# Optimization experiments

Hardware: AMD Instinct MI355X
Metric: run time of the kernel (lower is better)

The kernel has to match this reference:

```python
import jax, jax.numpy as jnp
import numpy as np

NUM_FIELDS = 32


def setup_inputs() -> dict:
    key = jax.random.key(0)
    x = jax.random.normal(key, (16384, NUM_FIELDS, 64), dtype=jnp.float32)
    return {"x": x}


def reference(x) -> jnp.ndarray:
    # x: [B, N, D] == list of N tensors [B,1,D] stacked on dim 1.
    # Original: for all i<j pairs, sum_d x[:,i,:]*x[:,j,:] -> [B, N(N-1)/2, 1].
    # Equivalent efficient form: Gram matrix x @ x^T, take strict upper triangle.
    n = x.shape[1]
    gram = jnp.einsum('bnd,bmd->bnm', x, x)  # [B, N, N]
    rows, cols = jnp.triu_indices(n, k=1)    # pair order matches i<j double loop
    inner_product = gram[:, rows, cols][..., None]  # [B, N(N-1)/2, 1]
    return inner_product
```

## Files before the change

### kernel.cpp

```cpp
#include <hip/hip_runtime.h>
#include <hip/hip_bf16.h>

#define NFIELDS 32
#define DDIM 64
#define NPAIR 496

typedef __attribute__((ext_vector_type(8))) __bf16 bf16x8;
typedef __attribute__((ext_vector_type(4))) float f32x4;

__device__ __forceinline__ int pair_idx(int i, int j) {
    return i * 31 - (i * (i - 1)) / 2 + (j - i - 1);
}

__global__ __launch_bounds__(256) void inner_product_kernel(
        const float* __restrict__ x, float* __restrict__ out, int nbatch) {
    const int gtid = blockIdx.x * blockDim.x + threadIdx.x;
    const int wave = gtid >> 6;
    const int lane = threadIdx.x & 63;
    if (wave >= nbatch) return;

    const float* xb = x + (size_t)wave * (NFIELDS * DDIM);
    const int r = lane & 15;
    const int g = lane >> 4;

    bf16x8 F[2][2];
#pragma unroll
    for (int rt = 0; rt < 2; ++rt) {
        const float* rowp = xb + (rt * 16 + r) * DDIM + g * 8;
#pragma unroll
        for (int kt = 0; kt < 2; ++kt) {
            const float4* p = reinterpret_cast<const float4*>(rowp + kt * 32);
            float4 a = p[0];
            float4 c = p[1];
            bf16x8 f;
            f[0] = (__bf16)a.x; f[1] = (__bf16)a.y; f[2] = (__bf16)a.z; f[3] = (__bf16)a.w;
            f[4] = (__bf16)c.x; f[5] = (__bf16)c.y; f[6] = (__bf16)c.z; f[7] = (__bf16)c.w;
            F[rt][kt] = f;
        }
    }

    f32x4 acc00 = {0.f, 0.f, 0.f, 0.f};
    f32x4 acc01 = {0.f, 0.f, 0.f, 0.f};
    f32x4 acc11 = {0.f, 0.f, 0.f, 0.f};
    acc00 = __builtin_amdgcn_mfma_f32_16x16x32_bf16(F[0][0], F[0][0], acc00, 0, 0, 0);
    acc00 = __builtin_amdgcn_mfma_f32_16x16x32_bf16(F[0][1], F[0][1], acc00, 0, 0, 0);
    acc01 = __builtin_amdgcn_mfma_f32_16x16x32_bf16(F[0][0], F[1][0], acc01, 0, 0, 0);
    acc01 = __builtin_amdgcn_mfma_f32_16x16x32_bf16(F[0][1], F[1][1], acc01, 0, 0, 0);
    acc11 = __builtin_amdgcn_mfma_f32_16x16x32_bf16(F[1][0], F[1][0], acc11, 0, 0, 0);
    acc11 = __builtin_amdgcn_mfma_f32_16x16x32_bf16(F[1][1], F[1][1], acc11, 0, 0, 0);

    float* ob = out + (size_t)wave * NPAIR;
    const int col = lane & 15;
    const int rowb = (lane >> 4) * 4;
#pragma unroll
    for (int v = 0; v < 4; ++v) {
        int i = rowb + v, j = col;
        if (j > i) ob[pair_idx(i, j)] = acc00[v];
    }
#pragma unroll
    for (int v = 0; v < 4; ++v) {
        int i = rowb + v, j = 16 + col;
        ob[pair_idx(i, j)] = acc01[v];
    }
#pragma unroll
    for (int v = 0; v < 4; ++v) {
        int i = 16 + rowb + v, j = 16 + col;
        if (j > i) ob[pair_idx(i, j)] = acc11[v];
    }
}

extern "C" void kernel_launch(void* const* d_in, const int* in_sizes, int n_in,
                              void* d_out, int out_size, void* d_ws, size_t ws_size,
                              hipStream_t stream) {
    const float* x = (const float*)d_in[0];
    float* out = (float*)d_out;
    const int nbatch = in_sizes[0] / (NFIELDS * DDIM);
    const int waves_per_block = 4;
    const int nblocks = (nbatch + waves_per_block - 1) / waves_per_block;
    inner_product_kernel<<<nblocks, 256, 0, stream>>>(x, out, nbatch);
}
```

Baseline: 31.78 us.

## Stage batch tile through LDS with direct global-to-LDS loads and nontemporal stores

Each wave now copies its 8 KB batch slice into LDS with fully coalesced 16-byte global_load_lds transfers, using an XOR swizzle to avoid bank conflicts. It then reads the fragments for the MFMA from LDS instead of issuing strided global loads. Output stores become nontemporal so they bypass cache pollution. The cost is 32 KB of LDS per block, which may limit occupancy, plus an extra LDS round trip on a memory-bound kernel.

Measured after the change: 35.23 us. +10.8%, slower.

```diff
diff --git a/kernel.cpp b/kernel.cpp
--- a/kernel.cpp
+++ b/kernel.cpp
@@ -4,6 +4,7 @@
 #define NFIELDS 32
 #define DDIM 64
 #define NPAIR 496
+#define BATCH_BYTES 8192
 
 typedef __attribute__((ext_vector_type(8))) __bf16 bf16x8;
 typedef __attribute__((ext_vector_type(4))) float f32x4;
@@ -12,26 +13,42 @@
     return i * 31 - (i * (i - 1)) / 2 + (j - i - 1);
 }
 
+__device__ __forceinline__ int swz(int b) {
+    return b ^ (((b >> 8) & 15) << 4);
+}
+
 __global__ __launch_bounds__(256) void inner_product_kernel(
         const float* __restrict__ x, float* __restrict__ out, int nbatch) {
-    const int gtid = blockIdx.x * blockDim.x + threadIdx.x;
-    const int wave = gtid >> 6;
+    __shared__ __align__(16) char smem_raw[4][BATCH_BYTES];
+    const int wib  = threadIdx.x >> 6;
     const int lane = threadIdx.x & 63;
+    const int wave = blockIdx.x * 4 + wib;
     if (wave >= nbatch) return;
 
-    const float* xb = x + (size_t)wave * (NFIELDS * DDIM);
+    const char* xb  = (const char*)(x + (size_t)wave * (NFIELDS * DDIM));
+    char*       lds = smem_raw[wib];
+
+#pragma unroll
+    for (int i = 0; i < 8; ++i) {
+        const int b  = i * 1024 + lane * 16;
+        const int sb = swz(b);
+        __builtin_amdgcn_global_load_lds(
+            (const __attribute__((address_space(1))) void*)(xb + sb),
+            (__attribute__((address_space(3))) void*)(lds + i * 1024),
+            16, 0, 0);
+    }
+    asm volatile("s_waitcnt vmcnt(0)" ::: "memory");
+
     const int r = lane & 15;
     const int g = lane >> 4;
-
     bf16x8 F[2][2];
 #pragma unroll
     for (int rt = 0; rt < 2; ++rt) {
-        const float* rowp = xb + (rt * 16 + r) * DDIM + g * 8;
 #pragma unroll
         for (int kt = 0; kt < 2; ++kt) {
-            const float4* p = reinterpret_cast<const float4*>(rowp + kt * 32);
-            float4 a = p[0];
-            float4 c = p[1];
+            const int b0 = (rt * 16 + r) * 256 + kt * 128 + g * 32;
+            const float4 a = *(const float4*)(lds + swz(b0));
+            const float4 c = *(const float4*)(lds + swz(b0 + 16));
             bf16x8 f;
             f[0] = (__bf16)a.x; f[1] = (__bf16)a.y; f[2] = (__bf16)a.z; f[3] = (__bf16)a.w;
             f[4] = (__bf16)c.x; f[5] = (__bf16)c.y; f[6] = (__bf16)c.z; f[7] = (__bf16)c.w;
@@ -50,22 +67,22 @@
     acc11 = __builtin_amdgcn_mfma_f32_16x16x32_bf16(F[1][1], F[1][1], acc11, 0, 0, 0);
 
     float* ob = out + (size_t)wave * NPAIR;
-    const int col = lane & 15;
+    const int col  = lane & 15;
     const int rowb = (lane >> 4) * 4;
 #pragma unroll
     for (int v = 0; v < 4; ++v) {
         int i = rowb + v, j = col;
-        if (j > i) ob[pair_idx(i, j)] = acc00[v];
+        if (j > i) __builtin_nontemporal_store(acc00[v], &ob[pair_idx(i, j)]);
     }
 #pragma unroll
     for (int v = 0; v < 4; ++v) {
         int i = rowb + v, j = 16 + col;
-        ob[pair_idx(i, j)] = acc01[v];
+        __builtin_nontemporal_store(acc01[v], &ob[pair_idx(i, j)]);
     }
 #pragma unroll
     for (int v = 0; v < 4; ++v) {
         int i = 16 + rowb + v, j = 16 + col;
-        if (j > i) ob[pair_idx(i, j)] = acc11[v];
+        if (j > i) __builtin_nontemporal_store(acc11[v], &ob[pair_idx(i, j)]);
     }
 }
 
@@ -75,7 +92,6 @@
     const float* x = (const float*)d_in[0];
     float* out = (float*)d_out;
     const int nbatch = in_sizes[0] / (NFIELDS * DDIM);
-    const int waves_per_block = 4;
-    const int nblocks = (nbatch + waves_per_block - 1) / waves_per_block;
+    const int nblocks = (nbatch + 3) / 4;
     inner_product_kernel<<<nblocks, 256, 0, stream>>>(x, out, nbatch);
 }
```
